# Performance work log

Hardware: AMD Instinct MI355X
Metric: run time of the kernel (lower is better)

Reference implementation:

```python
import jax, jax.numpy as jnp
import numpy as np


def setup_inputs() -> dict:
    key = jax.random.key(0)
    kq, kk, kv, km = jax.random.split(key, 4)
    B, H, N, D = 2, 16, 2048, 64
    q = jax.random.normal(kq, (B, H, N, D), dtype=jnp.float32)
    k = jax.random.normal(kk, (B, H, N, D), dtype=jnp.float32)
    v = jax.random.normal(kv, (B, H, N, D), dtype=jnp.float32)
    # mask > 0 means position is masked OUT (matches torch masked_fill(mask > 0, -max))
    mask = jax.random.randint(km, (B, N), 0, 2, dtype=jnp.int32)
    return {"q": q, "k": k, "v": v, "mask": mask}


def reference(q, k, v, mask):
    # q,k,v: [b,h,n,d]; mask: [b,j] with >0 = masked
    scale = q.shape[-1] ** -0.5
    sim = jnp.einsum('bhid,bhjd->bhij', q, k) * scale
    # l2_dist score modification: 2*qk*scale - ||q||^2 - ||k||^2
    q_sq = jnp.sum(q * q, axis=-1, keepdims=True)          # [b,h,i,1]
    k_sq = jnp.sum(k * k, axis=-1, keepdims=True)          # [b,h,j,1]
    sim = sim * 2 - q_sq - jnp.swapaxes(k_sq, -1, -2)       # [b,h,i,j]
    neg_max = -jnp.finfo(sim.dtype).max
    m = (mask > 0)[:, None, None, :]                        # [b,1,1,j]
    sim = jnp.where(m, neg_max, sim)
    attn = jax.nn.softmax(sim, axis=-1)
    out = jnp.einsum('bhij,bhjd->bhid', attn, v)
    return out
```

## Files before the change

### kernel.cpp

```cpp
#include <hip/hip_runtime.h>
#include <hip/hip_bf16.h>

#define NSEQ 2048
#define DD   64
#define HH   16
#define QT   128
#define KVB  64
#define NKV  (NSEQ / KVB)

typedef __attribute__((ext_vector_type(4)))  float f4;
typedef __attribute__((ext_vector_type(16))) float f32x16;
typedef __attribute__((ext_vector_type(8)))  short bf16x8;
typedef __attribute__((ext_vector_type(4)))  unsigned int u32x4;
typedef __attribute__((ext_vector_type(2)))  unsigned int u32x2;

#define QSCL  0.36067376022224085f
#define LOG2E 1.4426950408889634f
#define NEGBIG (-1.0e30f)
#define THR   8.0f

#define SWZ(row, q)  (((row) << 6) + ((((q) ^ ((row) & 7))) << 3))
#define SWZV(d, q)   (((d) << 6) + ((((q) ^ (((d) >> 2) & 7) ^ ((d) & 3))) << 3))

#if defined(__has_builtin)
#if __has_builtin(__builtin_amdgcn_exp2f)
#define EXP2F __builtin_amdgcn_exp2f
#endif
#if __has_builtin(__builtin_amdgcn_permlane32_swap)
#define HAVE_PLSWAP 1
#endif
#endif
#ifndef EXP2F
#define EXP2F exp2f
#endif

union bfu { u32x4 u; bf16x8 h; };

__device__ __forceinline__ unsigned cvtpk(float lo, float hi) {
    unsigned r;
    asm("v_cvt_pk_bf16_f32 %0, %1, %2" : "=v"(r) : "v"(lo), "v"(hi));
    return r;
}
template<int CTRL>
__device__ __forceinline__ float dppf(float x) {
    return __int_as_float(__builtin_amdgcn_update_dpp(
        0, __float_as_int(x), CTRL, 0xF, 0xF, true));
}
__device__ __forceinline__ float cross_max(float x) {
#ifdef HAVE_PLSWAP
    u32x2 r = __builtin_amdgcn_permlane32_swap(__float_as_uint(x), __float_as_uint(x),
                                               false, false);
    return fmaxf(__uint_as_float(r[0]), __uint_as_float(r[1]));
#else
    return fmaxf(x, __shfl_xor(x, 32));
#endif
}
__device__ __forceinline__ float cross_add(float x) {
#ifdef HAVE_PLSWAP
    u32x2 r = __builtin_amdgcn_permlane32_swap(__float_as_uint(x), __float_as_uint(x),
                                               false, false);
    return __uint_as_float(r[0]) + __uint_as_float(r[1]);
#else
    return x + __shfl_xor(x, 32);
#endif
}
__device__ __forceinline__ void pairmix(unsigned A, unsigned B,
                                        unsigned& d0, unsigned& d2, bool hi) {
#ifdef HAVE_PLSWAP
    u32x2 r = __builtin_amdgcn_permlane32_swap(A, B, false, false);
    d0 = r[0]; d2 = r[1];
#else
    unsigned v = hi ? A : B;
    unsigned x = (unsigned)__shfl_xor((int)v, 32);
    d0 = hi ? x : A;
    d2 = hi ? B : x;
#endif
}

__global__ __launch_bounds__(256, 2)
void attend_kernel(const float* __restrict__ qg, const float* __restrict__ kg,
                   const float* __restrict__ vg, const int* __restrict__ maskg,
                   float* __restrict__ outg)
{
    __shared__ __align__(16) unsigned short Ks[2][KVB * DD];
    __shared__ __align__(16) unsigned short Vt[3][KVB * DD];
    __shared__ __align__(16) float bias_s[2][KVB];

    const int t    = threadIdx.x;
    const int w    = t >> 6;
    const int lane = t & 63;
    const int c5   = lane & 31;
    const int g2   = lane >> 5;

    const int p     = blockIdx.x;
    const int bh    = (p & 7) * 4 + ((p >> 3) >> 4);
    const int qtile = (p >> 3) & 15;
    const int b     = bh >> 4;

    const size_t base = (size_t)bh * NSEQ * DD;
    const float* kp = kg + base;
    const float* vp = vg + base;
    const int*   mp = maskg + b * NSEQ;

    bfu qf[4];
    {
        const float* qp = qg + base + (size_t)(qtile*QT + w*32 + c5) * DD;
        #pragma unroll
        for (int ck = 0; ck < 4; ++ck) {
            f4 a  = *(const f4*)(qp + ck*16 + g2*8);
            f4 bb = *(const f4*)(qp + ck*16 + g2*8 + 4);
            qf[ck].u = (u32x4){ cvtpk(a[0]*QSCL,  a[1]*QSCL),  cvtpk(a[2]*QSCL,  a[3]*QSCL),
                                cvtpk(bb[0]*QSCL, bb[1]*QSCL), cvtpk(bb[2]*QSCL, bb[3]*QSCL) };
        }
    }

    f32x16 acc0, acc1;
    #pragma unroll
    for (int r = 0; r < 16; ++r) { acc0[r] = 0.f; acc1[r] = 0.f; }
    float m_run = NEGBIG, l_run = 0.f;

    const bool isK = (w < 2);
    const int  jK  = t >> 1;
    const int  kq0 = (t & 1) * 4;
    const int  uv  = t & 127;
    const int  dq  = uv & 15;
    const int  jq  = uv >> 4;

    f4  st[8];
    int mr = 0;

    auto loadTile = [&](int gt) {
        const int j0 = gt * KVB;
        if (isK) {
            const float* src = kp + (size_t)(j0 + jK) * DD + kq0 * 8;
            #pragma unroll
            for (int i2 = 0; i2 < 8; ++i2) st[i2] = ((const f4*)src)[i2];
            mr = mp[j0 + jK];
        } else {
            #pragma unroll
            for (int i2 = 0; i2 < 8; ++i2)
                st[i2] = *(const f4*)(vp + (size_t)(j0 + jq*8 + i2) * DD + dq*4);
        }
    };

    auto stageTile = [&](int ksel, int vsel) {
        if (isK) {
            float sq = 0.f;
            #pragma unroll
            for (int i2 = 0; i2 < 8; ++i2)
                sq += st[i2][0]*st[i2][0] + st[i2][1]*st[i2][1]
                    + st[i2][2]*st[i2][2] + st[i2][3]*st[i2][3];
            sq += dppf<0xB1>(sq);
            if ((t & 1) == 0) bias_s[ksel][jK] = (mr > 0) ? NEGBIG : -sq * LOG2E;
            #pragma unroll
            for (int s2 = 0; s2 < 4; ++s2) {
                u32x4 kk = (u32x4){ cvtpk(st[2*s2][0],   st[2*s2][1]),
                                    cvtpk(st[2*s2][2],   st[2*s2][3]),
                                    cvtpk(st[2*s2+1][0], st[2*s2+1][1]),
                                    cvtpk(st[2*s2+1][2], st[2*s2+1][3]) };
                *(u32x4*)&Ks[ksel][SWZ(jK, kq0 + s2)] = kk;
            }
        } else {
            #pragma unroll
            for (int cc = 0; cc < 4; ++cc) {
                int d = dq*4 + cc;
                u32x4 tv = (u32x4){ cvtpk(st[0][cc], st[1][cc]),
                                    cvtpk(st[2][cc], st[3][cc]),
                                    cvtpk(st[4][cc], st[5][cc]),
                                    cvtpk(st[6][cc], st[7][cc]) };
                *(u32x4*)&Vt[vsel][SWZV(d, jq)] = tv;
            }
        }
    };

    loadTile(0);
    stageTile(0, 0);
    loadTile(1);
    __syncthreads();

    int vc = 0;
    for (int kt = 0; kt < NKV; ++kt) {
        const int kc = kt & 1;
        int vn = vc + 1; if (vn == 3) vn = 0;

        if (kt + 1 < NKV) stageTile(kc ^ 1, vn);
        if (kt + 2 < NKV) loadTile(kt + 2);

        f32x16 s01[2];
        #pragma unroll
        for (int jt = 0; jt < 2; ++jt) {
            f4 b4[4];
            #pragma unroll
            for (int q = 0; q < 4; ++q)
                b4[q] = *(const f4*)&bias_s[kc][32*jt + 8*q + 4*g2];
            f32x16 sc;
            #pragma unroll
            for (int r = 0; r < 16; ++r) sc[r] = b4[r>>2][r&3];
            __builtin_amdgcn_s_setprio(1);
            #pragma unroll
            for (int ck = 0; ck < 4; ++ck) {
                bfu kb;
                kb.u = *(const u32x4*)&Ks[kc][SWZ(32*jt + c5, 2*ck + g2)];
                sc = __builtin_amdgcn_mfma_f32_32x32x16_bf16(kb.h, qf[ck].h, sc, 0, 0, 0);
            }
            __builtin_amdgcn_s_setprio(0);
            s01[jt] = sc;
        }

        float pmax;
        {
            float mm[8];
            #pragma unroll
            for (int i2 = 0; i2 < 8; ++i2)
                mm[i2] = fmaxf(fmaxf(s01[0][2*i2], s01[0][2*i2+1]),
                               fmaxf(s01[1][2*i2], s01[1][2*i2+1]));
            float ma = fmaxf(fmaxf(mm[0], mm[1]), fmaxf(mm[2], mm[3]));
            float mb = fmaxf(fmaxf(mm[4], mm[5]), fmaxf(mm[6], mm[7]));
            pmax = fmaxf(ma, mb);
        }
        pmax = cross_max(pmax);
        if (!__all(pmax <= m_run + THR)) {
            float mn = fmaxf(m_run, pmax);
            float corr = EXP2F(m_run - mn);
            m_run = mn;
            l_run *= corr;
            #pragma unroll
            for (int r = 0; r < 16; ++r) { acc0[r] *= corr; acc1[r] *= corr; }
        }

        unsigned Wp[16];
        float ls0 = 0.f, ls1 = 0.f;
        #pragma unroll
        for (int jt = 0; jt < 2; ++jt) {
            #pragma unroll
            for (int m = 0; m < 8; ++m) {
                float e0 = EXP2F(s01[jt][2*m]   - m_run);
                float e1 = EXP2F(s01[jt][2*m+1] - m_run);
                if (m & 1) ls1 += e0 + e1; else ls0 += e0 + e1;
                Wp[jt*8 + m] = cvtpk(e0, e1);
            }
        }
        l_run += ls0 + ls1;

        __syncthreads();

        const bool hi = (g2 != 0);
        __builtin_amdgcn_s_setprio(1);
        #pragma unroll
        for (int ck = 0; ck < 4; ++ck) {
            const int bs = (ck >> 1) * 8 + 4 * (ck & 1);
            unsigned d00, d20, d01, d21;
            pairmix(Wp[bs],   Wp[bs+2], d00, d20, hi);
            pairmix(Wp[bs+1], Wp[bs+3], d01, d21, hi);
            bfu pb;
            pb.u = (u32x4){ d00, d01, d20, d21 };
            bfu va0, va1;
            va0.u = *(const u32x4*)&Vt[vc][SWZV(     c5, 2*ck + g2)];
            va1.u = *(const u32x4*)&Vt[vc][SWZV(32 + c5, 2*ck + g2)];
            acc0 = __builtin_amdgcn_mfma_f32_32x32x16_bf16(va0.h, pb.h, acc0, 0, 0, 0);
            acc1 = __builtin_amdgcn_mfma_f32_32x32x16_bf16(va1.h, pb.h, acc1, 0, 0, 0);
        }
        __builtin_amdgcn_s_setprio(0);

        vc = vn;
    }

    l_run = cross_add(l_run);
    float inv = 1.0f / l_run;
    float* op = outg + base + (size_t)(qtile*QT + w*32 + c5) * DD;
    #pragma unroll
    for (int dt = 0; dt < 2; ++dt) {
        const f32x16 A = dt ? acc1 : acc0;
        #pragma unroll
        for (int q = 0; q < 4; ++q) {
            f4 o = { A[4*q]*inv, A[4*q+1]*inv, A[4*q+2]*inv, A[4*q+3]*inv };
            *(f4*)(op + 32*dt + 8*q + 4*g2) = o;
        }
    }
}

extern "C" void kernel_launch(void* const* d_in, const int* in_sizes, int n_in,
                              void* d_out, int out_size, void* d_ws, size_t ws_size,
                              hipStream_t stream) {
    const float* q    = (const float*)d_in[0];
    const float* k    = (const float*)d_in[1];
    const float* v    = (const float*)d_in[2];
    const int*   mask = (const int*)d_in[3];
    float* out = (float*)d_out;
    attend_kernel<<<dim3(512), dim3(256), 0, stream>>>(q, k, v, mask, out);
}
```

Measured before the change: 65.34 us.

## Single-buffer V tile and stage V after PV with extra barriers

Replaces the triple-buffered V shared tile with a single buffer. K staging stays at the top of the loop, while V staging is moved after the PV MFMAs and placed between two block barriers. The partial row sum is now cross-lane reduced every iteration instead of once at the end. This cuts LDS use, which may help occupancy, but adds a barrier per iteration and serializes V staging with compute, so V writes no longer overlap the QK phase.

```diff
diff --git a/kernel.cpp b/kernel.cpp
--- a/kernel.cpp
+++ b/kernel.cpp
@@ -83,7 +83,7 @@
                    float* __restrict__ outg)
 {
     __shared__ __align__(16) unsigned short Ks[2][KVB * DD];
-    __shared__ __align__(16) unsigned short Vt[3][KVB * DD];
+    __shared__ __align__(16) unsigned short Vt[KVB * DD];
     __shared__ __align__(16) float bias_s[2][KVB];
 
     const int t    = threadIdx.x;
@@ -143,48 +143,47 @@
         }
     };
 
-    auto stageTile = [&](int ksel, int vsel) {
-        if (isK) {
-            float sq = 0.f;
-            #pragma unroll
-            for (int i2 = 0; i2 < 8; ++i2)
-                sq += st[i2][0]*st[i2][0] + st[i2][1]*st[i2][1]
-                    + st[i2][2]*st[i2][2] + st[i2][3]*st[i2][3];
-            sq += dppf<0xB1>(sq);
-            if ((t & 1) == 0) bias_s[ksel][jK] = (mr > 0) ? NEGBIG : -sq * LOG2E;
-            #pragma unroll
-            for (int s2 = 0; s2 < 4; ++s2) {
-                u32x4 kk = (u32x4){ cvtpk(st[2*s2][0],   st[2*s2][1]),
-                                    cvtpk(st[2*s2][2],   st[2*s2][3]),
-                                    cvtpk(st[2*s2+1][0], st[2*s2+1][1]),
-                                    cvtpk(st[2*s2+1][2], st[2*s2+1][3]) };
-                *(u32x4*)&Ks[ksel][SWZ(jK, kq0 + s2)] = kk;
-            }
-        } else {
-            #pragma unroll
-            for (int cc = 0; cc < 4; ++cc) {
-                int d = dq*4 + cc;
-                u32x4 tv = (u32x4){ cvtpk(st[0][cc], st[1][cc]),
-                                    cvtpk(st[2][cc], st[3][cc]),
-                                    cvtpk(st[4][cc], st[5][cc]),
-                                    cvtpk(st[6][cc], st[7][cc]) };
-                *(u32x4*)&Vt[vsel][SWZV(d, jq)] = tv;
-            }
+    auto stageK = [&](int ksel) {
+        float sq = 0.f;
+        #pragma unroll
+        for (int i2 = 0; i2 < 8; ++i2)
+            sq += st[i2][0]*st[i2][0] + st[i2][1]*st[i2][1]
+                + st[i2][2]*st[i2][2] + st[i2][3]*st[i2][3];
+        sq += dppf<0xB1>(sq);
+        if ((t & 1) == 0) bias_s[ksel][jK] = (mr > 0) ? NEGBIG : -sq * LOG2E;
+        #pragma unroll
+        for (int s2 = 0; s2 < 4; ++s2) {
+            u32x4 kk = (u32x4){ cvtpk(st[2*s2][0],   st[2*s2][1]),
+                                cvtpk(st[2*s2][2],   st[2*s2][3]),
+                                cvtpk(st[2*s2+1][0], st[2*s2+1][1]),
+                                cvtpk(st[2*s2+1][2], st[2*s2+1][3]) };
+            *(u32x4*)&Ks[ksel][SWZ(jK, kq0 + s2)] = kk;
         }
     };
+    auto stageV = [&]() {
+        #pragma unroll
+        for (int cc = 0; cc < 4; ++cc) {
+            int d = dq*4 + cc;
+            u32x4 tv = (u32x4){ cvtpk(st[0][cc], st[1][cc]),
+                                cvtpk(st[2][cc], st[3][cc]),
+                                cvtpk(st[4][cc], st[5][cc]),
+                                cvtpk(st[6][cc], st[7][cc]) };
+            *(u32x4*)&Vt[SWZV(d, jq)] = tv;
+        }
+    };
 
     loadTile(0);
-    stageTile(0, 0);
+    if (isK) stageK(0); else stageV();
     loadTile(1);
     __syncthreads();
 
-    int vc = 0;
     for (int kt = 0; kt < NKV; ++kt) {
         const int kc = kt & 1;
-        int vn = vc + 1; if (vn == 3) vn = 0;
-
-        if (kt + 1 < NKV) stageTile(kc ^ 1, vn);
-        if (kt + 2 < NKV) loadTile(kt + 2);
+
+        if (isK && kt + 1 < NKV) {
+            stageK(kc ^ 1);
+            if (kt + 2 < NKV) loadTile(kt + 2);
+        }
 
         f32x16 s01[2];
         #pragma unroll
@@ -240,9 +239,7 @@
                 Wp[jt*8 + m] = cvtpk(e0, e1);
             }
         }
-        l_run += ls0 + ls1;
-
-        __syncthreads();
+        l_run += cross_add(ls0 + ls1);
 
         const bool hi = (g2 != 0);
         __builtin_amdgcn_s_setprio(1);
@@ -255,17 +252,23 @@
             bfu pb;
             pb.u = (u32x4){ d00, d01, d20, d21 };
             bfu va0, va1;
-            va0.u = *(const u32x4*)&Vt[vc][SWZV(     c5, 2*ck + g2)];
-            va1.u = *(const u32x4*)&Vt[vc][SWZV(32 + c5, 2*ck + g2)];
+            va0.u = *(const u32x4*)&Vt[SWZV(     c5, 2*ck + g2)];
+            va1.u = *(const u32x4*)&Vt[SWZV(32 + c5, 2*ck + g2)];
             acc0 = __builtin_amdgcn_mfma_f32_32x32x16_bf16(va0.h, pb.h, acc0, 0, 0, 0);
             acc1 = __builtin_amdgcn_mfma_f32_32x32x16_bf16(va1.h, pb.h, acc1, 0, 0, 0);
         }
         __builtin_amdgcn_s_setprio(0);
 
-        vc = vn;
+        __syncthreads();
+
+        if (!isK && kt + 1 < NKV) {
+            stageV();
+            if (kt + 2 < NKV) loadTile(kt + 2);
+        }
+
+        __syncthreads();
     }
 
-    l_run = cross_add(l_run);
     float inv = 1.0f / l_run;
     float* op = outg + base + (size_t)(qtile*QT + w*32 + c5) * DD;
     #pragma unroll
```

Measured after the change: 65.31 us. About the same (-0.1%).
